# Optimization experiments

Measured on AMD Instinct MI355X. Metric: run time of the kernel, lower is better.

## Reference

```python
import jax, jax.numpy as jnp
import numpy as np
from jax import lax

EPS = 1e-12


def _conv_block(x, w, scale, bias, pool):
    # x: (N, Cin, H, W), w: (Cout, Cin, 3, 3). BN in eval mode folded into scale/bias.
    y = lax.conv_general_dilated(x, w, window_strides=(1, 1), padding='SAME',
                                 dimension_numbers=('NCHW', 'OIHW', 'NCHW'))
    y = y * scale[None, :, None, None] + bias[None, :, None, None]
    y = jax.nn.relu(y)
    if pool:
        y = lax.reduce_window(y, -jnp.inf, lax.max, (1, 1, 2, 2), (1, 1, 2, 2), 'VALID')
    return y


def _encoder(x, w1, s1, b1, w2, s2, b2, w3, s3, b3, w4, s4, b4):
    x = _conv_block(x, w1, s1, b1, True)
    x = _conv_block(x, w2, s2, b2, True)
    x = _conv_block(x, w3, s3, b3, False)
    x = _conv_block(x, w4, s4, b4, False)
    return x  # (N, 64, 21, 21)


def _l2norm(x, axis):
    n = jnp.sqrt(jnp.sum(x * x, axis=axis, keepdims=True))
    return x / jnp.maximum(n, EPS)


def setup_inputs() -> dict:
    key = jax.random.key(0)
    ks = jax.random.split(key, 8)
    B, NQ, Way, Shot, C, H, W = 2, 75, 5, 5, 3, 84, 84
    D = 64
    inp = {
        'query': jax.random.normal(ks[0], (B, NQ, C, H, W), jnp.float32),
        'support': jax.random.normal(ks[1], (B, Way, Shot, C, H, W), jnp.float32),
        'w1': jax.random.normal(ks[2], (D, C, 3, 3), jnp.float32) * 0.1,
        'w2': jax.random.normal(ks[3], (D, D, 3, 3), jnp.float32) * 0.05,
        'w3': jax.random.normal(ks[4], (D, D, 3, 3), jnp.float32) * 0.05,
        'w4': jax.random.normal(ks[5], (D, D, 3, 3), jnp.float32) * 0.05,
    }
    for i in range(1, 5):
        inp[f's{i}'] = jnp.ones((D,), jnp.float32)
        inp[f'b{i}'] = jnp.zeros((D,), jnp.float32)
    return inp


def reference(query, support, w1, s1, b1, w2, s2, b2, w3, s3, b3, w4, s4, b4):
    B, NQ, C, H, W = query.shape
    _, Way, Shot, _, _, _ = support.shape
    q_flat = query.reshape(B * NQ, C, H, W)
    s_flat = support.reshape(B * Way * Shot, C, H, W)
    q_feat = _encoder(q_flat, w1, s1, b1, w2, s2, b2, w3, s3, b3, w4, s4, b4)
    s_feat = _encoder(s_flat, w1, s1, b1, w2, s2, b2, w3, s3, b3, w4, s4, b4)
    D, h, w = q_feat.shape[1], q_feat.shape[2], q_feat.shape[3]
    HW = h * w
    q_local = _l2norm(q_feat.reshape(B, NQ, D, HW), axis=2)            # (B,NQ,D,HW)
    s_local = s_feat.reshape(B, Way, Shot, D, HW).mean(axis=2)          # mean over shots
    s_local = _l2norm(s_local, axis=2)                                  # (B,Way,D,HW)
    # all pairwise local cosine similarities, batched in one einsum
    sim = jnp.einsum('bqdm,bcdn->bqcmn', q_local, s_local)              # (B,NQ,Way,HW,HW)
    best = sim.max(axis=-1)                                             # best match per query descriptor
    scores = best.mean(axis=-1)                                         # (B,NQ,Way)
    return scores.reshape(B * NQ, Way)
```

## Files before the change

kernel.cpp:

```cpp
#include <hip/hip_runtime.h>

#define EPS 1e-12f

#define NIMG   200
#define NQIMG  150
#define BDIM   2
#define NQ     75
#define WAY    5
#define SHOT   5
#define DCH    64
#define H1     84
#define H2     42
#define H3     21
#define HW2    1764
#define HW3    441
#define PH     86
#define PSZ    7396
#define SST    448

#define PAD_BLKS  17335
#define W1_BLKS   8
#define W_BLKS    432

typedef __attribute__((ext_vector_type(8))) short bf16x8;
typedef __attribute__((ext_vector_type(4))) float f32x4;

__device__ __forceinline__ unsigned short f2bf(float f) {
    unsigned u = __float_as_uint(f);
    u += 0x7fffu + ((u >> 16) & 1u);
    return (unsigned short)(u >> 16);
}
__device__ __forceinline__ float bf2f(unsigned short h) {
    return __uint_as_float(((unsigned)h) << 16);
}
__device__ __forceinline__ int swz(int pix, int c) {
    return pix * 128 + ((c ^ ((pix >> 1) & 7)) << 4);
}

__global__ __launch_bounds__(256) void prep(
    const float* __restrict__ qin, const float* __restrict__ sin_,
    const float* __restrict__ w1, const float* __restrict__ s1,
    const float* __restrict__ w2, const float* __restrict__ s2,
    const float* __restrict__ w3, const float* __restrict__ s3,
    const float* __restrict__ w4, const float* __restrict__ s4,
    unsigned short* __restrict__ pad, unsigned short* __restrict__ p1,
    unsigned short* __restrict__ p2, unsigned short* __restrict__ p3,
    unsigned short* __restrict__ p4)
{
    int blk = blockIdx.x;
    if (blk < PAD_BLKS) {
        int idx = blk * 256 + threadIdx.x;
        if (idx >= NIMG * 3 * PSZ) return;
        int img = idx / (3 * PSZ);
        int rem = idx % (3 * PSZ);
        int ci = rem / PSZ, p = rem % PSZ;
        int iy = p / PH, ix = p % PH;
        float v = 0.f;
        if (iy >= 1 && iy <= H1 && ix >= 1 && ix <= H1) {
            const float* src = (img < NQIMG) ? (qin + (size_t)img * 3 * H1 * H1)
                                             : (sin_ + (size_t)(img - NQIMG) * 3 * H1 * H1);
            v = src[(size_t)ci * H1 * H1 + (iy - 1) * H1 + (ix - 1)];
        }
        pad[idx] = f2bf(v);
    } else if (blk < PAD_BLKS + W1_BLKS) {
        int idx = (blk - PAD_BLKS) * 256 + threadIdx.x;
        int j = idx & 7, lane = (idx >> 3) & 63, mt = idx >> 9;
        int co = (mt << 4) + (lane & 15);
        int k = ((lane >> 4) << 3) + j;
        float v = 0.f;
        if (k < 27) {
            int ci = k / 9, s = k % 9;
            v = w1[(co * 3 + ci) * 9 + s] * s1[co];
        }
        p1[idx] = f2bf(v);
    } else {
        int idx = (blk - PAD_BLKS - W1_BLKS) * 256 + threadIdx.x;
        int which = idx / 36864;
        int r = idx % 36864;
        int j = r & 7, lane = (r >> 3) & 63, mt = (r >> 9) & 3, t = (r >> 11) & 1, s = r >> 12;
        int co = (mt << 4) + (lane & 15);
        int ci = (t << 5) + ((lane >> 4) << 3) + j;
        const float* w = (which == 0) ? w2 : (which == 1) ? w3 : w4;
        const float* sc = (which == 0) ? s2 : (which == 1) ? s3 : s4;
        unsigned short* p = (which == 0) ? p2 : (which == 1) ? p3 : p4;
        p[r] = f2bf(w[(co * 64 + ci) * 9 + s] * sc[co]);
    }
}

__global__ __launch_bounds__(256) void conv1_mfma(
    const unsigned short* __restrict__ pad,
    const unsigned short* __restrict__ wp1,
    const float* __restrict__ bias,
    unsigned short* __restrict__ out)
{
    int img = blockIdx.x / 7, seg = blockIdx.x % 7;
    int tid = threadIdx.x;
    __shared__ unsigned short strip[3 * 14 * 86];

    const unsigned* srcd = (const unsigned*)pad;
    size_t ibase = (size_t)img * 3 * (PSZ / 2);
    #pragma unroll
    for (int it = 0; it < 8; it++) {
        int i = it * 256 + tid;
        if (i < 1806) {
            int ci = i / 602, r = i % 602;
            ((unsigned*)strip)[i] = srcd[ibase + ci * (PSZ / 2) + 516 * seg + r];
        }
    }
    __syncthreads();

    int wv = tid >> 6, lane = tid & 63;
    int lc = lane & 15, kg = lane >> 4;

    const bf16x8* wvv = (const bf16x8*)wp1;
    bf16x8 a0 = wvv[lane];
    bf16x8 a1 = wvv[64 + lane];
    bf16x8 a2 = wvv[128 + lane];
    bf16x8 a3 = wvv[192 + lane];

    int off[8];
    #pragma unroll
    for (int j = 0; j < 8; j++) {
        int k = (kg << 3) + j;
        int kk = k < 27 ? k : 0;
        int ci = kk / 9, s = kk % 9;
        off[j] = ci * 1204 + (s / 3) * 86 + (s % 3);
    }

    f32x4 bini[4];
    #pragma unroll
    for (int mt = 0; mt < 4; mt++) {
        float4 bq = *reinterpret_cast<const float4*>(bias + (mt << 4) + (kg << 2));
        bini[mt] = (f32x4){bq.x, bq.y, bq.z, bq.w};
    }

    #pragma unroll
    for (int it = 0; it < 4; it++) {
        int pl = it * 64 + wv * 16 + lc;
        bool valid = pl < 252;
        int plc = valid ? pl : 251;
        int pyl = plc / 42, pxl = plc % 42;
        int base = pyl * 172 + 2 * pxl;

        bf16x8 b[4];
        #pragma unroll
        for (int j = 0; j < 8; j++) {
            int a = base + off[j];
            b[0][j] = (short)strip[a];
            b[1][j] = (short)strip[a + 1];
            b[2][j] = (short)strip[a + 86];
            b[3][j] = (short)strip[a + 87];
        }

        f32x4 acc[4][4];
        #pragma unroll
        for (int mt = 0; mt < 4; mt++)
            #pragma unroll
            for (int sub = 0; sub < 4; sub++)
                acc[mt][sub] = bini[mt];
        #pragma unroll
        for (int sub = 0; sub < 4; sub++) {
            acc[0][sub] = __builtin_amdgcn_mfma_f32_16x16x32_bf16(a0, b[sub], acc[0][sub], 0, 0, 0);
            acc[1][sub] = __builtin_amdgcn_mfma_f32_16x16x32_bf16(a1, b[sub], acc[1][sub], 0, 0, 0);
            acc[2][sub] = __builtin_amdgcn_mfma_f32_16x16x32_bf16(a2, b[sub], acc[2][sub], 0, 0, 0);
            acc[3][sub] = __builtin_amdgcn_mfma_f32_16x16x32_bf16(a3, b[sub], acc[3][sub], 0, 0, 0);
        }

        if (valid) {
            int p = seg * 252 + pl;
            #pragma unroll
            for (int mt = 0; mt < 4; mt++) {
                unsigned short uo[4];
                #pragma unroll
                for (int r = 0; r < 4; r++) {
                    float m = fmaxf(fmaxf(acc[mt][0][r], acc[mt][1][r]),
                                    fmaxf(acc[mt][2][r], acc[mt][3][r]));
                    uo[r] = f2bf(fmaxf(m, 0.f));
                }
                uint2 pk;
                pk.x = (unsigned)uo[0] | ((unsigned)uo[1] << 16);
                pk.y = (unsigned)uo[2] | ((unsigned)uo[3] << 16);
                *reinterpret_cast<uint2*>(out + ((size_t)img * HW2 + p) * DCH + (mt << 4) + (kg << 2)) = pk;
            }
        }
    }
}

__global__ __launch_bounds__(256) void conv2_mfma_pool(
    const unsigned short* __restrict__ act,
    const unsigned short* __restrict__ wp,
    const float* __restrict__ bias,
    unsigned short* __restrict__ out)
{
    int img = blockIdx.x / 7, tg = blockIdx.x % 7;
    int tid = threadIdx.x;
    __shared__ unsigned short lds[8 * 44 * DCH];

    const unsigned short* ab = act + (size_t)img * HW2 * DCH;
    int ybase = 6 * tg - 1;
    #pragma unroll
    for (int it = 0; it < 11; it++) {
        int idx = it * 256 + tid;
        int pix = idx >> 3, c = idx & 7;
        int r = pix / 44, xx = pix % 44;
        int y = ybase + r, x = xx - 1;
        bf16x8 v = (bf16x8)(short)0;
        if ((unsigned)y < (unsigned)H2 && (unsigned)x < (unsigned)H2)
            v = *(const bf16x8*)(ab + ((size_t)(y * H2 + x)) * DCH + (c << 3));
        *(bf16x8*)((char*)lds + swz(pix, c)) = v;
    }
    __syncthreads();

    int wv = tid >> 6, lane = tid & 63;
    int lc = lane & 15, kg = lane >> 4;
    int p_local = wv * 16 + lc;
    bool valid = p_local < 63;
    int pl = valid ? p_local : 62;
    int pyl = pl / 21, pxl = pl % 21;
    int pixc[4];
    #pragma unroll
    for (int sub = 0; sub < 4; sub++)
        pixc[sub] = (2 * pyl + (sub >> 1) + 1) * 44 + (2 * pxl + (sub & 1) + 1);

    f32x4 bini[4];
    #pragma unroll
    for (int mt = 0; mt < 4; mt++) {
        float4 bq = *reinterpret_cast<const float4*>(bias + (mt << 4) + (kg << 2));
        bini[mt] = (f32x4){bq.x, bq.y, bq.z, bq.w};
    }

    const bf16x8* wvv = (const bf16x8*)wp;
    f32x4 acc[4][4];
    #pragma unroll
    for (int i = 0; i < 4; i++)
        #pragma unroll
        for (int j = 0; j < 4; j++)
            acc[i][j] = bini[i];

    for (int s = 0; s < 9; s++) {
        int offs = (s / 3 - 1) * 44 + (s % 3 - 1);
        #pragma unroll
        for (int t = 0; t < 2; t++) {
            int fbase = ((s * 2 + t) * 4) << 6;
            bf16x8 a0 = wvv[fbase + lane];
            bf16x8 a1 = wvv[fbase + 64 + lane];
            bf16x8 a2 = wvv[fbase + 128 + lane];
            bf16x8 a3 = wvv[fbase + 192 + lane];
            int c = (t << 2) + kg;
            bf16x8 b[4];
            #pragma unroll
            for (int sub = 0; sub < 4; sub++) {
                int pix = pixc[sub] + offs;
                b[sub] = *(const bf16x8*)((const char*)lds + swz(pix, c));
            }
            #pragma unroll
            for (int sub = 0; sub < 4; sub++) {
                acc[0][sub] = __builtin_amdgcn_mfma_f32_16x16x32_bf16(a0, b[sub], acc[0][sub], 0, 0, 0);
                acc[1][sub] = __builtin_amdgcn_mfma_f32_16x16x32_bf16(a1, b[sub], acc[1][sub], 0, 0, 0);
                acc[2][sub] = __builtin_amdgcn_mfma_f32_16x16x32_bf16(a2, b[sub], acc[2][sub], 0, 0, 0);
                acc[3][sub] = __builtin_amdgcn_mfma_f32_16x16x32_bf16(a3, b[sub], acc[3][sub], 0, 0, 0);
            }
        }
    }

    if (!valid) return;
    int p = tg * 63 + p_local;
    #pragma unroll
    for (int mt = 0; mt < 4; mt++) {
        unsigned short uo[4];
        #pragma unroll
        for (int r = 0; r < 4; r++) {
            float m = fmaxf(fmaxf(acc[mt][0][r], acc[mt][1][r]),
                            fmaxf(acc[mt][2][r], acc[mt][3][r]));
            uo[r] = f2bf(fmaxf(m, 0.f));
        }
        uint2 pk;
        pk.x = (unsigned)uo[0] | ((unsigned)uo[1] << 16);
        pk.y = (unsigned)uo[2] | ((unsigned)uo[3] << 16);
        *reinterpret_cast<uint2*>(out + ((size_t)img * HW3 + p) * DCH + (mt << 4) + (kg << 2)) = pk;
    }
}

__global__ __launch_bounds__(256) void conv34_fused(
    const unsigned short* __restrict__ act,
    const unsigned short* __restrict__ wp3, const unsigned short* __restrict__ wp4,
    const float* __restrict__ b3, const float* __restrict__ b4,
    unsigned short* __restrict__ a4out,
    unsigned short* __restrict__ qlout)
{
    int img = blockIdx.x;
    int tid = threadIdx.x;
    __shared__ unsigned short lds[529 * DCH];

    const unsigned short* ab = act + (size_t)img * HW3 * DCH;
    #pragma unroll
    for (int it = 0; it < 17; it++) {
        int idx = it * 256 + tid;
        if (idx < 529 * 8) {
            int pix = idx >> 3, c = idx & 7;
            int r = pix / 23, xx = pix % 23;
            int y = r - 1, x = xx - 1;
            bf16x8 v = (bf16x8)(short)0;
            if ((unsigned)y < (unsigned)H3 && (unsigned)x < (unsigned)H3)
                v = *(const bf16x8*)(ab + ((size_t)(y * H3 + x)) * DCH + (c << 3));
            *(bf16x8*)((char*)lds + swz(pix, c)) = v;
        }
    }
    __syncthreads();

    int wv = tid >> 6, lane = tid & 63;
    int lc = lane & 15, kg = lane >> 4;
    int pixBase[7];
    bool pv[7];
    #pragma unroll
    for (int i = 0; i < 7; i++) {
        int p = (wv * 7 + i) * 16 + lc;
        pv[i] = p < HW3;
        int pc = pv[i] ? p : HW3 - 1;
        pixBase[i] = (pc / 21) * 23 + (pc % 21);
    }

    f32x4 bini[4];
    #pragma unroll
    for (int mt = 0; mt < 4; mt++) {
        float4 bq = *reinterpret_cast<const float4*>(b3 + (mt << 4) + (kg << 2));
        bini[mt] = (f32x4){bq.x, bq.y, bq.z, bq.w};
    }

    f32x4 acc[7][4];
    #pragma unroll
    for (int i = 0; i < 7; i++)
        #pragma unroll
        for (int m = 0; m < 4; m++)
            acc[i][m] = bini[m];

    const bf16x8* wv3 = (const bf16x8*)wp3;
    for (int s = 0; s < 9; s++) {
        int offs = (s / 3) * 23 + (s % 3);
        #pragma unroll
        for (int t = 0; t < 2; t++) {
            int fbase = ((s * 2 + t) * 4) << 6;
            bf16x8 a0 = wv3[fbase + lane];
            bf16x8 a1 = wv3[fbase + 64 + lane];
            bf16x8 a2 = wv3[fbase + 128 + lane];
            bf16x8 a3 = wv3[fbase + 192 + lane];
            int c = (t << 2) + kg;
            #pragma unroll
            for (int i = 0; i < 7; i++) {
                int pix = pixBase[i] + offs;
                bf16x8 bb = *(const bf16x8*)((const char*)lds + swz(pix, c));
                acc[i][0] = __builtin_amdgcn_mfma_f32_16x16x32_bf16(a0, bb, acc[i][0], 0, 0, 0);
                acc[i][1] = __builtin_amdgcn_mfma_f32_16x16x32_bf16(a1, bb, acc[i][1], 0, 0, 0);
                acc[i][2] = __builtin_amdgcn_mfma_f32_16x16x32_bf16(a2, bb, acc[i][2], 0, 0, 0);
                acc[i][3] = __builtin_amdgcn_mfma_f32_16x16x32_bf16(a3, bb, acc[i][3], 0, 0, 0);
            }
        }
    }

    __syncthreads();

    #pragma unroll
    for (int i = 0; i < 7; i++) {
        if (!pv[i]) continue;
        int pix = pixBase[i] + 24;
        #pragma unroll
        for (int mt = 0; mt < 4; mt++) {
            unsigned short uo[4];
            #pragma unroll
            for (int r = 0; r < 4; r++)
                uo[r] = f2bf(fmaxf(acc[i][mt][r], 0.f));
            uint2 pk;
            pk.x = (unsigned)uo[0] | ((unsigned)uo[1] << 16);
            pk.y = (unsigned)uo[2] | ((unsigned)uo[3] << 16);
            int c = (mt << 1) + (kg >> 1);
            *(uint2*)((char*)lds + swz(pix, c) + ((kg & 1) << 3)) = pk;
        }
    }
    #pragma unroll
    for (int it = 0; it < 3; it++) {
        int idx = it * 256 + tid;
        if (idx < 704) {
            int j = idx >> 3, c = idx & 7;
            int pix;
            if (j < 23)      pix = j;
            else if (j < 46) pix = 506 + (j - 23);
            else { int k = j - 46; pix = (1 + (k >> 1)) * 23 + (k & 1) * 22; }
            *(bf16x8*)((char*)lds + swz(pix, c)) = (bf16x8)(short)0;
        }
    }
    __syncthreads();

    #pragma unroll
    for (int mt = 0; mt < 4; mt++) {
        float4 bq = *reinterpret_cast<const float4*>(b4 + (mt << 4) + (kg << 2));
        bini[mt] = (f32x4){bq.x, bq.y, bq.z, bq.w};
    }
    #pragma unroll
    for (int i = 0; i < 7; i++)
        #pragma unroll
        for (int m = 0; m < 4; m++)
            acc[i][m] = bini[m];

    const bf16x8* wv4 = (const bf16x8*)wp4;
    for (int s = 0; s < 9; s++) {
        int offs = (s / 3) * 23 + (s % 3);
        #pragma unroll
        for (int t = 0; t < 2; t++) {
            int fbase = ((s * 2 + t) * 4) << 6;
            bf16x8 a0 = wv4[fbase + lane];
            bf16x8 a1 = wv4[fbase + 64 + lane];
            bf16x8 a2 = wv4[fbase + 128 + lane];
            bf16x8 a3 = wv4[fbase + 192 + lane];
            int c = (t << 2) + kg;
            #pragma unroll
            for (int i = 0; i < 7; i++) {
                int pix = pixBase[i] + offs;
                bf16x8 bb = *(const bf16x8*)((const char*)lds + swz(pix, c));
                acc[i][0] = __builtin_amdgcn_mfma_f32_16x16x32_bf16(a0, bb, acc[i][0], 0, 0, 0);
                acc[i][1] = __builtin_amdgcn_mfma_f32_16x16x32_bf16(a1, bb, acc[i][1], 0, 0, 0);
                acc[i][2] = __builtin_amdgcn_mfma_f32_16x16x32_bf16(a2, bb, acc[i][2], 0, 0, 0);
                acc[i][3] = __builtin_amdgcn_mfma_f32_16x16x32_bf16(a3, bb, acc[i][3], 0, 0, 0);
            }
        }
    }

    if (img < NQIMG) {
        #pragma unroll
        for (int i = 0; i < 7; i++) {
            float v[4][4];
            float ssq = 0.f;
            #pragma unroll
            for (int mt = 0; mt < 4; mt++)
                #pragma unroll
                for (int r = 0; r < 4; r++) {
                    float x = fmaxf(acc[i][mt][r], 0.f);
                    v[mt][r] = x;
                    ssq = fmaf(x, x, ssq);
                }
            ssq += __shfl_xor(ssq, 16, 64);
            ssq += __shfl_xor(ssq, 32, 64);
            float inv = 1.f / fmaxf(sqrtf(ssq), EPS);
            if (!pv[i]) continue;
            int p = (wv * 7 + i) * 16 + lc;
            #pragma unroll
            for (int mt = 0; mt < 4; mt++) {
                unsigned short uo[4];
                #pragma unroll
                for (int r = 0; r < 4; r++)
                    uo[r] = f2bf(v[mt][r] * inv);
                uint2 pk;
                pk.x = (unsigned)uo[0] | ((unsigned)uo[1] << 16);
                pk.y = (unsigned)uo[2] | ((unsigned)uo[3] << 16);
                *reinterpret_cast<uint2*>(qlout + ((size_t)img * HW3 + p) * DCH + (mt << 4) + (kg << 2)) = pk;
            }
        }
    } else {
        #pragma unroll
        for (int mt = 0; mt < 4; mt++) {
            #pragma unroll
            for (int i = 0; i < 7; i++) {
                if (!pv[i]) continue;
                int p = (wv * 7 + i) * 16 + lc;
                unsigned short uo[4];
                #pragma unroll
                for (int r = 0; r < 4; r++)
                    uo[r] = f2bf(fmaxf(acc[i][mt][r], 0.f));
                uint2 pk;
                pk.x = (unsigned)uo[0] | ((unsigned)uo[1] << 16);
                pk.y = (unsigned)uo[2] | ((unsigned)uo[3] << 16);
                *reinterpret_cast<uint2*>(a4out + ((size_t)img * HW3 + p) * DCH + (mt << 4) + (kg << 2)) = pk;
            }
        }
    }
}

__global__ __launch_bounds__(256) void s_mean_norm(
    const unsigned short* __restrict__ feat, unsigned short* __restrict__ s_local)
{
    int idx = blockIdx.x * 256 + threadIdx.x;
    if (idx >= BDIM * WAY * SST) return;
    int hw = idx % SST;
    int bc = idx / SST;
    bf16x8* o = (bf16x8*)(s_local + (size_t)idx * DCH);
    if (hw >= HW3) {
        #pragma unroll
        for (int g = 0; g < 8; g++) o[g] = (bf16x8)(short)0;
        return;
    }
    int img0 = NQIMG + bc * SHOT;
    float v[DCH];
    #pragma unroll
    for (int d = 0; d < DCH; d++) v[d] = 0.f;
    for (int sh = 0; sh < SHOT; sh++) {
        const bf16x8* f = (const bf16x8*)(feat + ((size_t)(img0 + sh) * HW3 + hw) * DCH);
        #pragma unroll
        for (int g = 0; g < 8; g++) {
            bf16x8 x = f[g];
            #pragma unroll
            for (int j = 0; j < 8; j++)
                v[g * 8 + j] += bf2f((unsigned short)x[j]);
        }
    }
    float ss = 0.f;
    #pragma unroll
    for (int d = 0; d < DCH; d++) {
        v[d] *= (1.f / SHOT);
        ss = fmaf(v[d], v[d], ss);
    }
    float inv = 1.f / fmaxf(sqrtf(ss), EPS);
    #pragma unroll
    for (int g = 0; g < 8; g++) {
        bf16x8 pk;
        #pragma unroll
        for (int j = 0; j < 8; j++) pk[j] = (short)f2bf(v[g * 8 + j] * inv);
        o[g] = pk;
    }
}

__global__ __launch_bounds__(256) void sim_mfma(
    const unsigned short* __restrict__ qloc,
    const unsigned short* __restrict__ sloc,
    float* __restrict__ out)
{
    int blk = blockIdx.x;
    int imgq = blk / WAY, way = blk % WAY;
    int b = imgq / NQ;
    const unsigned short* qp = qloc + (size_t)imgq * HW3 * DCH;
    const unsigned short* sp = sloc + (size_t)(b * WAY + way) * SST * DCH;

    int tid = threadIdx.x;
    int wv = tid >> 6, lane = tid & 63;
    int lc = lane & 15, kg = lane >> 4;
    int mt0 = wv * 7;

    bf16x8 qa0[7], qa1[7];
    #pragma unroll
    for (int i = 0; i < 7; i++) {
        const unsigned short* qrow = qp + (size_t)((mt0 + i) * 16 + lc) * DCH + (kg << 3);
        qa0[i] = *(const bf16x8*)(qrow);
        qa1[i] = *(const bf16x8*)(qrow + 32);
    }
    f32x4 rmax[7];
    #pragma unroll
    for (int i = 0; i < 7; i++)
        rmax[i] = (f32x4){-1e30f, -1e30f, -1e30f, -1e30f};

    const f32x4 z4 = (f32x4){0.f, 0.f, 0.f, 0.f};
    const unsigned short* sbase = sp + (size_t)lc * DCH + (kg << 3);

    for (int t = 0; t < 13; t++) {
        const unsigned short* r0 = sbase + (size_t)(2 * t) * 16 * DCH;
        const unsigned short* r1 = r0 + 16 * DCH;
        bf16x8 sA0 = *(const bf16x8*)(r0);
        bf16x8 sA1 = *(const bf16x8*)(r0 + 32);
        bf16x8 sB0 = *(const bf16x8*)(r1);
        bf16x8 sB1 = *(const bf16x8*)(r1 + 32);
        #pragma unroll
        for (int i = 0; i < 7; i++) {
            f32x4 aA = __builtin_amdgcn_mfma_f32_16x16x32_bf16(qa0[i], sA0, z4, 0, 0, 0);
            aA = __builtin_amdgcn_mfma_f32_16x16x32_bf16(qa1[i], sA1, aA, 0, 0, 0);
            f32x4 aB = __builtin_amdgcn_mfma_f32_16x16x32_bf16(qa0[i], sB0, z4, 0, 0, 0);
            aB = __builtin_amdgcn_mfma_f32_16x16x32_bf16(qa1[i], sB1, aB, 0, 0, 0);
            #pragma unroll
            for (int r = 0; r < 4; r++)
                rmax[i][r] = fmaxf(rmax[i][r], fmaxf(aA[r], aB[r]));
        }
    }
    {
        const unsigned short* r0 = sbase + (size_t)26 * 16 * DCH;
        const unsigned short* r1 = r0 + 16 * DCH;
        bf16x8 sA0 = *(const bf16x8*)(r0);
        bf16x8 sA1 = *(const bf16x8*)(r0 + 32);
        bf16x8 sB0 = *(const bf16x8*)(r1);
        bf16x8 sB1 = *(const bf16x8*)(r1 + 32);
        bool nval = (432 + lc) < HW3;
        #pragma unroll
        for (int i = 0; i < 7; i++) {
            f32x4 aA = __builtin_amdgcn_mfma_f32_16x16x32_bf16(qa0[i], sA0, z4, 0, 0, 0);
            aA = __builtin_amdgcn_mfma_f32_16x16x32_bf16(qa1[i], sA1, aA, 0, 0, 0);
            f32x4 aB = __builtin_amdgcn_mfma_f32_16x16x32_bf16(qa0[i], sB0, z4, 0, 0, 0);
            aB = __builtin_amdgcn_mfma_f32_16x16x32_bf16(qa1[i], sB1, aB, 0, 0, 0);
            #pragma unroll
            for (int r = 0; r < 4; r++)
                rmax[i][r] = fmaxf(rmax[i][r], fmaxf(aA[r], nval ? aB[r] : -1e30f));
        }
    }

    float msum = 0.f;
    #pragma unroll
    for (int i = 0; i < 7; i++) {
        #pragma unroll
        for (int r = 0; r < 4; r++) {
            float v = rmax[i][r];
            v = fmaxf(v, __shfl_xor(v, 1, 64));
            v = fmaxf(v, __shfl_xor(v, 2, 64));
            v = fmaxf(v, __shfl_xor(v, 4, 64));
            v = fmaxf(v, __shfl_xor(v, 8, 64));
            int m = (mt0 + i) * 16 + (kg << 2) + r;
            if (lc == 0 && m < HW3) msum += v;
        }
    }
    #pragma unroll
    for (int off = 32; off > 0; off >>= 1)
        msum += __shfl_xor(msum, off, 64);
    __shared__ float red[4];
    if (lane == 0) red[wv] = msum;
    __syncthreads();
    if (tid == 0)
        out[(size_t)imgq * WAY + way] = (red[0] + red[1] + red[2] + red[3]) * (1.f / HW3);
}

extern "C" void kernel_launch(void* const* d_in, const int* in_sizes, int n_in,
                              void* d_out, int out_size, void* d_ws, size_t ws_size,
                              hipStream_t stream) {
    const float* query   = (const float*)d_in[0];
    const float* support = (const float*)d_in[1];
    const float* w1 = (const float*)d_in[2];
    const float* w2 = (const float*)d_in[3];
    const float* w3 = (const float*)d_in[4];
    const float* w4 = (const float*)d_in[5];
    const float* s1 = (const float*)d_in[6];
    const float* b1 = (const float*)d_in[7];
    const float* s2 = (const float*)d_in[8];
    const float* b2 = (const float*)d_in[9];
    const float* s3 = (const float*)d_in[10];
    const float* b3 = (const float*)d_in[11];
    const float* s4 = (const float*)d_in[12];
    const float* b4 = (const float*)d_in[13];
    float* out = (float*)d_out;

    char* ws = (char*)d_ws;
    unsigned short* A1  = (unsigned short*)(ws);
    unsigned short* A2  = (unsigned short*)(ws + 45158400);
    unsigned short* A4  = (unsigned short*)(ws + 56448000);
    unsigned short* QL  = (unsigned short*)(ws + 67737600);
    unsigned short* SL  = (unsigned short*)(ws + 76204800);
    unsigned short* WP2 = (unsigned short*)(ws + 76778240);
    unsigned short* WP3 = (unsigned short*)(ws + 76851968);
    unsigned short* WP4 = (unsigned short*)(ws + 76925696);
    unsigned short* WP1 = (unsigned short*)(ws + 76999424);
    unsigned short* PAD = (unsigned short*)(ws + 77003520);

    prep<<<PAD_BLKS + W1_BLKS + W_BLKS, 256, 0, stream>>>(
        query, support, w1, s1, w2, s2, w3, s3, w4, s4, PAD, WP1, WP2, WP3, WP4);

    conv1_mfma<<<NIMG * 7, 256, 0, stream>>>(PAD, WP1, b1, A1);
    conv2_mfma_pool<<<NIMG * 7, 256, 0, stream>>>(A1, WP2, b2, A2);
    conv34_fused<<<NIMG, 256, 0, stream>>>(A2, WP3, WP4, b3, b4, A4, QL);

    s_mean_norm<<<(BDIM * WAY * SST + 255) / 256, 256, 0, stream>>>(A4, SL);

    sim_mfma<<<NQIMG * WAY, 256, 0, stream>>>(QL, SL, out);
}
```

Before: 136.7 us.

## Fuse input padding/bf16 conversion into conv1 and unroll sim loop by four

Drops the separate pass that wrote a padded bf16 copy of all input images. conv1 now reads the fp32 inputs directly, applies zero padding with bounds checks and converts to bf16 while filling its shared strip. This removes a full write and re-read of the padded buffer, at the cost of more per-element index math and twice as many 4-byte loads per strip in conv1. Separately, the similarity kernel now processes four support tiles per iteration instead of two, giving more independent MFMA chains in flight at the cost of more registers.

Result: slower. 142.6 us (+4.3%).

```diff
diff --git a/kernel.cpp b/kernel.cpp
--- a/kernel.cpp
+++ b/kernel.cpp
@@ -12,13 +12,11 @@
 #define H1     84
 #define H2     42
 #define H3     21
+#define HW1    7056
 #define HW2    1764
 #define HW3    441
-#define PH     86
-#define PSZ    7396
 #define SST    448
 
-#define PAD_BLKS  17335
 #define W1_BLKS   8
 #define W_BLKS    432
 
@@ -38,32 +36,16 @@
 }
 
 __global__ __launch_bounds__(256) void prep(
-    const float* __restrict__ qin, const float* __restrict__ sin_,
     const float* __restrict__ w1, const float* __restrict__ s1,
     const float* __restrict__ w2, const float* __restrict__ s2,
     const float* __restrict__ w3, const float* __restrict__ s3,
     const float* __restrict__ w4, const float* __restrict__ s4,
-    unsigned short* __restrict__ pad, unsigned short* __restrict__ p1,
-    unsigned short* __restrict__ p2, unsigned short* __restrict__ p3,
-    unsigned short* __restrict__ p4)
+    unsigned short* __restrict__ p1, unsigned short* __restrict__ p2,
+    unsigned short* __restrict__ p3, unsigned short* __restrict__ p4)
 {
     int blk = blockIdx.x;
-    if (blk < PAD_BLKS) {
+    if (blk < W1_BLKS) {
         int idx = blk * 256 + threadIdx.x;
-        if (idx >= NIMG * 3 * PSZ) return;
-        int img = idx / (3 * PSZ);
-        int rem = idx % (3 * PSZ);
-        int ci = rem / PSZ, p = rem % PSZ;
-        int iy = p / PH, ix = p % PH;
-        float v = 0.f;
-        if (iy >= 1 && iy <= H1 && ix >= 1 && ix <= H1) {
-            const float* src = (img < NQIMG) ? (qin + (size_t)img * 3 * H1 * H1)
-                                             : (sin_ + (size_t)(img - NQIMG) * 3 * H1 * H1);
-            v = src[(size_t)ci * H1 * H1 + (iy - 1) * H1 + (ix - 1)];
-        }
-        pad[idx] = f2bf(v);
-    } else if (blk < PAD_BLKS + W1_BLKS) {
-        int idx = (blk - PAD_BLKS) * 256 + threadIdx.x;
         int j = idx & 7, lane = (idx >> 3) & 63, mt = idx >> 9;
         int co = (mt << 4) + (lane & 15);
         int k = ((lane >> 4) << 3) + j;
@@ -74,7 +56,7 @@
         }
         p1[idx] = f2bf(v);
     } else {
-        int idx = (blk - PAD_BLKS - W1_BLKS) * 256 + threadIdx.x;
+        int idx = (blk - W1_BLKS) * 256 + threadIdx.x;
         int which = idx / 36864;
         int r = idx % 36864;
         int j = r & 7, lane = (r >> 3) & 63, mt = (r >> 9) & 3, t = (r >> 11) & 1, s = r >> 12;
@@ -88,7 +70,7 @@
 }
 
 __global__ __launch_bounds__(256) void conv1_mfma(
-    const unsigned short* __restrict__ pad,
+    const float* __restrict__ qin, const float* __restrict__ sin_,
     const unsigned short* __restrict__ wp1,
     const float* __restrict__ bias,
     unsigned short* __restrict__ out)
@@ -97,14 +79,19 @@
     int tid = threadIdx.x;
     __shared__ unsigned short strip[3 * 14 * 86];
 
-    const unsigned* srcd = (const unsigned*)pad;
-    size_t ibase = (size_t)img * 3 * (PSZ / 2);
-    #pragma unroll
-    for (int it = 0; it < 8; it++) {
+    const float* src = (img < NQIMG) ? (qin + (size_t)img * 3 * HW1)
+                                     : (sin_ + (size_t)(img - NQIMG) * 3 * HW1);
+    #pragma unroll
+    for (int it = 0; it < 15; it++) {
         int i = it * 256 + tid;
-        if (i < 1806) {
-            int ci = i / 602, r = i % 602;
-            ((unsigned*)strip)[i] = srcd[ibase + ci * (PSZ / 2) + 516 * seg + r];
+        if (i < 3612) {
+            int ci = i / 1204, rem = i % 1204;
+            int r = rem / 86, xx = rem % 86;
+            int y = 12 * seg + r - 1, x = xx - 1;
+            float v = 0.f;
+            if ((unsigned)y < (unsigned)H1 && (unsigned)x < (unsigned)H1)
+                v = src[(size_t)ci * HW1 + y * H1 + x];
+            strip[i] = f2bf(v);
         }
     }
     __syncthreads();
@@ -548,41 +535,50 @@
     const f32x4 z4 = (f32x4){0.f, 0.f, 0.f, 0.f};
     const unsigned short* sbase = sp + (size_t)lc * DCH + (kg << 3);
 
-    for (int t = 0; t < 13; t++) {
-        const unsigned short* r0 = sbase + (size_t)(2 * t) * 16 * DCH;
-        const unsigned short* r1 = r0 + 16 * DCH;
-        bf16x8 sA0 = *(const bf16x8*)(r0);
-        bf16x8 sA1 = *(const bf16x8*)(r0 + 32);
-        bf16x8 sB0 = *(const bf16x8*)(r1);
-        bf16x8 sB1 = *(const bf16x8*)(r1 + 32);
+    for (int g = 0; g < 6; g++) {
+        bf16x8 s0[4], s1[4];
+        #pragma unroll
+        for (int u = 0; u < 4; u++) {
+            const unsigned short* r0 = sbase + (size_t)(4 * g + u) * 16 * DCH;
+            s0[u] = *(const bf16x8*)(r0);
+            s1[u] = *(const bf16x8*)(r0 + 32);
+        }
         #pragma unroll
         for (int i = 0; i < 7; i++) {
-            f32x4 aA = __builtin_amdgcn_mfma_f32_16x16x32_bf16(qa0[i], sA0, z4, 0, 0, 0);
-            aA = __builtin_amdgcn_mfma_f32_16x16x32_bf16(qa1[i], sA1, aA, 0, 0, 0);
-            f32x4 aB = __builtin_amdgcn_mfma_f32_16x16x32_bf16(qa0[i], sB0, z4, 0, 0, 0);
-            aB = __builtin_amdgcn_mfma_f32_16x16x32_bf16(qa1[i], sB1, aB, 0, 0, 0);
+            f32x4 a[4];
+            #pragma unroll
+            for (int u = 0; u < 4; u++) {
+                a[u] = __builtin_amdgcn_mfma_f32_16x16x32_bf16(qa0[i], s0[u], z4, 0, 0, 0);
+                a[u] = __builtin_amdgcn_mfma_f32_16x16x32_bf16(qa1[i], s1[u], a[u], 0, 0, 0);
+            }
             #pragma unroll
             for (int r = 0; r < 4; r++)
-                rmax[i][r] = fmaxf(rmax[i][r], fmaxf(aA[r], aB[r]));
+                rmax[i][r] = fmaxf(rmax[i][r],
+                                   fmaxf(fmaxf(a[0][r], a[1][r]), fmaxf(a[2][r], a[3][r])));
         }
     }
     {
-        const unsigned short* r0 = sbase + (size_t)26 * 16 * DCH;
-        const unsigned short* r1 = r0 + 16 * DCH;
-        bf16x8 sA0 = *(const bf16x8*)(r0);
-        bf16x8 sA1 = *(const bf16x8*)(r0 + 32);
-        bf16x8 sB0 = *(const bf16x8*)(r1);
-        bf16x8 sB1 = *(const bf16x8*)(r1 + 32);
+        bf16x8 s0[4], s1[4];
+        #pragma unroll
+        for (int u = 0; u < 4; u++) {
+            const unsigned short* r0 = sbase + (size_t)(24 + u) * 16 * DCH;
+            s0[u] = *(const bf16x8*)(r0);
+            s1[u] = *(const bf16x8*)(r0 + 32);
+        }
         bool nval = (432 + lc) < HW3;
         #pragma unroll
         for (int i = 0; i < 7; i++) {
-            f32x4 aA = __builtin_amdgcn_mfma_f32_16x16x32_bf16(qa0[i], sA0, z4, 0, 0, 0);
-            aA = __builtin_amdgcn_mfma_f32_16x16x32_bf16(qa1[i], sA1, aA, 0, 0, 0);
-            f32x4 aB = __builtin_amdgcn_mfma_f32_16x16x32_bf16(qa0[i], sB0, z4, 0, 0, 0);
-            aB = __builtin_amdgcn_mfma_f32_16x16x32_bf16(qa1[i], sB1, aB, 0, 0, 0);
+            f32x4 a[4];
+            #pragma unroll
+            for (int u = 0; u < 4; u++) {
+                a[u] = __builtin_amdgcn_mfma_f32_16x16x32_bf16(qa0[i], s0[u], z4, 0, 0, 0);
+                a[u] = __builtin_amdgcn_mfma_f32_16x16x32_bf16(qa1[i], s1[u], a[u], 0, 0, 0);
+            }
             #pragma unroll
             for (int r = 0; r < 4; r++)
-                rmax[i][r] = fmaxf(rmax[i][r], fmaxf(aA[r], nval ? aB[r] : -1e30f));
+                rmax[i][r] = fmaxf(rmax[i][r],
+                                   fmaxf(fmaxf(a[0][r], a[1][r]),
+                                         fmaxf(a[2][r], nval ? a[3][r] : -1e30f)));
         }
     }
 
@@ -639,12 +635,11 @@
     unsigned short* WP3 = (unsigned short*)(ws + 76851968);
     unsigned short* WP4 = (unsigned short*)(ws + 76925696);
     unsigned short* WP1 = (unsigned short*)(ws + 76999424);
-    unsigned short* PAD = (unsigned short*)(ws + 77003520);
-
-    prep<<<PAD_BLKS + W1_BLKS + W_BLKS, 256, 0, stream>>>(
-        query, support, w1, s1, w2, s2, w3, s3, w4, s4, PAD, WP1, WP2, WP3, WP4);
-
-    conv1_mfma<<<NIMG * 7, 256, 0, stream>>>(PAD, WP1, b1, A1);
+
+    prep<<<W1_BLKS + W_BLKS, 256, 0, stream>>>(
+        w1, s1, w2, s2, w3, s3, w4, s4, WP1, WP2, WP3, WP4);
+
+    conv1_mfma<<<NIMG * 7, 256, 0, stream>>>(query, support, WP1, b1, A1);
     conv2_mfma_pool<<<NIMG * 7, 256, 0, stream>>>(A1, WP2, b2, A2);
     conv34_fused<<<NIMG, 256, 0, stream>>>(A2, WP3, WP4, b3, b4, A4, QL);
 
```
